# Optimization experiments

Hardware: AMD Instinct MI355X
Metric: run time of the kernel (lower is better)

## Reference

```python
import jax, jax.numpy as jnp
import numpy as np

B, D, H = 8192, 1024, 1024

def setup_inputs() -> dict:
    key = jax.random.key(0)
    ks = jax.random.split(key, 7)
    s_x = 1.0 / np.sqrt(D)
    s_h = 1.0 / np.sqrt(H)
    return {
        "e_t": jax.random.normal(ks[0], (B, D), jnp.float32),
        "h_prev": jax.random.normal(ks[1], (B, H), jnp.float32),
        "c_prev": jax.random.normal(ks[2], (B, H), jnp.float32),
        # gates concatenated in order (f, i, o, c), each block of size H
        "W_x": jax.random.uniform(ks[3], (4 * H, D), jnp.float32, -s_x, s_x),
        "b_x": jax.random.uniform(ks[4], (4 * H,), jnp.float32, -s_x, s_x),
        "W_h": jax.random.uniform(ks[5], (4 * H, H), jnp.float32, -s_h, s_h),
        "b_h": jax.random.uniform(ks[6], (4 * H,), jnp.float32, -s_h, s_h),
        "b_extra": jnp.zeros((4 * H,), jnp.float32),  # the b_f/b_i/b_o/b_c Parameters
    }

def reference(e_t, h_prev, c_prev, W_x, b_x, W_h, b_h, b_extra):
    # two fused GEMMs: [B,D]@[D,4H] and [B,H]@[H,4H]
    z = (jnp.einsum('bd,gd->bg', e_t, W_x)
         + jnp.einsum('bh,gh->bg', h_prev, W_h)
         + b_x + b_h + b_extra)  # [B, 4H]
    zf, zi, zo, zc = jnp.split(z, 4, axis=-1)
    g_t = jax.nn.sigmoid(zf)   # forget gate
    p_t = jax.nn.sigmoid(zi)   # input gate
    q_t = jax.nn.sigmoid(zo)   # output gate
    m_t_hat = jnp.tanh(zc)     # candidate cell
    c_t = g_t * c_prev + p_t * m_t_hat
    h_t = q_t * jnp.tanh(c_t)
    return (h_t, c_t)
```

## Files before the change

### kernel.cpp

```cpp
#include <hip/hip_runtime.h>
#include <stdint.h>

#define B_ROWS 8192
#define DH     1024
#define KTOT   2048
#define NTOT   4096

typedef __attribute__((ext_vector_type(8))) __bf16 bf16x8;
typedef __attribute__((ext_vector_type(4))) float  f32x4;

__device__ __forceinline__ unsigned short f2bf(float f) {
    unsigned int u = __float_as_uint(f);
    u += 0x7FFFu + ((u >> 16) & 1u);
    return (unsigned short)(u >> 16);
}

__device__ __forceinline__ float fast_sigmoid(float x) {
    return 1.0f / (1.0f + __expf(-x));
}
__device__ __forceinline__ float fast_tanh(float x) {
    float e = __expf(fminf(-2.0f * x, 80.0f));
    return (1.0f - e) / (1.0f + e);
}

#define NBLK_A (B_ROWS)
#define NBLK_W (NTOT)
#define NBLK_BIAS (NTOT / 256)

__global__ __launch_bounds__(256) void pack_all(const float* __restrict__ e_t,
                                                const float* __restrict__ h_prev,
                                                const float* __restrict__ W_x,
                                                const float* __restrict__ W_h,
                                                const float* __restrict__ b_x,
                                                const float* __restrict__ b_h,
                                                const float* __restrict__ b_e,
                                                unsigned short* __restrict__ A_cat,
                                                unsigned short* __restrict__ W_cat,
                                                float* __restrict__ bias) {
    const int blk = blockIdx.x;
    const int t   = threadIdx.x;
    if (blk < NBLK_A + NBLK_W) {
        const float* src0;
        unsigned short* dst;
        int row;
        if (blk < NBLK_A) {
            row = blk;
            dst = A_cat + (size_t)row * KTOT;
            int c8 = t << 3;
            src0 = (c8 < DH) ? (e_t + (size_t)row * DH + c8)
                             : (h_prev + (size_t)row * DH + (c8 - DH));
        } else {
            row = blk - NBLK_A;
            int gate = (row >> 4) & 3;
            int h    = (row >> 6) * 16 + (row & 15);
            int srow = gate * DH + h;
            dst = W_cat + (size_t)row * KTOT;
            int c8 = t << 3;
            src0 = (c8 < DH) ? (W_x + (size_t)srow * DH + c8)
                             : (W_h + (size_t)srow * DH + (c8 - DH));
        }
        float4 f0 = ((const float4*)src0)[0];
        float4 f1 = ((const float4*)src0)[1];
        uint4 o;
        o.x = (unsigned)f2bf(f0.x) | ((unsigned)f2bf(f0.y) << 16);
        o.y = (unsigned)f2bf(f0.z) | ((unsigned)f2bf(f0.w) << 16);
        o.z = (unsigned)f2bf(f1.x) | ((unsigned)f2bf(f1.y) << 16);
        o.w = (unsigned)f2bf(f1.z) | ((unsigned)f2bf(f1.w) << 16);
        *(uint4*)(dst + t * 8) = o;
    } else {
        int gp = (blk - NBLK_A - NBLK_W) * 256 + t;
        int gate = (gp >> 4) & 3;
        int h    = (gp >> 6) * 16 + (gp & 15);
        int g    = gate * DH + h;
        bias[gp] = b_x[g] + b_h[g] + b_e[g];
    }
}


#define GLL(srcp, dstp) \
    __builtin_amdgcn_global_load_lds( \
        (const __attribute__((address_space(1))) void*)(srcp), \
        (__attribute__((address_space(3))) void*)(dstp), 16, 0, 0)

#define STAGE_HALF(g, buf, h, kt) do { \
    GLL((g) + ((size_t)((h) * 128)      * KTOT) + (size_t)(kt) * 64, (buf) + (((h) * 128)      + w8) * 128); \
    GLL((g) + ((size_t)((h) * 128 + 64) * KTOT) + (size_t)(kt) * 64, (buf) + (((h) * 128 + 64) + w8) * 128); \
} while (0)

#define SB() __builtin_amdgcn_sched_barrier(0)

template <int MODE>
__device__ __forceinline__ void do_tile(
    int kt,
    unsigned char* As_cur, unsigned char* Bs_cur,
    const unsigned short* __restrict__ gA, const unsigned short* __restrict__ gB,
    int w8, int rowA, int rowB, int xg0, int xg1,
    f32x4 (&acc)[8][4])
{
    bf16x8 afl[4][2], afh[4][2], bfl[2][2], bfh[2][2];

#pragma unroll
    for (int mi = 0; mi < 4; ++mi) {
        afl[mi][0] = *(const bf16x8*)(As_cur + rowA + mi * 2048 + xg0);
        afl[mi][1] = *(const bf16x8*)(As_cur + rowA + mi * 2048 + xg1);
    }
#pragma unroll
    for (int ni = 0; ni < 2; ++ni) {
        bfl[ni][0] = *(const bf16x8*)(Bs_cur + rowB + ni * 2048 + xg0);
        bfl[ni][1] = *(const bf16x8*)(Bs_cur + rowB + ni * 2048 + xg1);
    }
    SB();
#pragma unroll
    for (int ni = 0; ni < 2; ++ni) {
        bfh[ni][0] = *(const bf16x8*)(Bs_cur + rowB + (2 + ni) * 2048 + xg0);
        bfh[ni][1] = *(const bf16x8*)(Bs_cur + rowB + (2 + ni) * 2048 + xg1);
    }
    SB();
#pragma unroll
    for (int mi = 0; mi < 4; ++mi) {
        afh[mi][0] = *(const bf16x8*)(As_cur + rowA + (4 + mi) * 2048 + xg0);
        afh[mi][1] = *(const bf16x8*)(As_cur + rowA + (4 + mi) * 2048 + xg1);
    }
    SB();

    asm volatile("s_waitcnt lgkmcnt(12)" ::: "memory");
    SB();
    __builtin_amdgcn_s_setprio(1);
#pragma unroll
    for (int mi = 0; mi < 4; ++mi)
#pragma unroll
        for (int ni = 0; ni < 2; ++ni) {
            acc[mi][ni] = __builtin_amdgcn_mfma_f32_16x16x32_bf16(afl[mi][0], bfl[ni][0], acc[mi][ni], 0, 0, 0);
            acc[mi][ni] = __builtin_amdgcn_mfma_f32_16x16x32_bf16(afl[mi][1], bfl[ni][1], acc[mi][ni], 0, 0, 0);
        }
    __builtin_amdgcn_s_setprio(0);
    SB();

    asm volatile("s_waitcnt lgkmcnt(8)" ::: "memory");
    SB();
    __builtin_amdgcn_s_setprio(1);
#pragma unroll
    for (int mi = 0; mi < 4; ++mi)
#pragma unroll
        for (int ni = 0; ni < 2; ++ni) {
            acc[mi][2 + ni] = __builtin_amdgcn_mfma_f32_16x16x32_bf16(afl[mi][0], bfh[ni][0], acc[mi][2 + ni], 0, 0, 0);
            acc[mi][2 + ni] = __builtin_amdgcn_mfma_f32_16x16x32_bf16(afl[mi][1], bfh[ni][1], acc[mi][2 + ni], 0, 0, 0);
        }
    __builtin_amdgcn_s_setprio(0);
    SB();

    asm volatile("s_waitcnt lgkmcnt(0)" ::: "memory");
    SB();
    if constexpr (MODE == 2) {
        __builtin_amdgcn_s_barrier();
        SB();
        STAGE_HALF(gB, Bs_cur, 0, kt + 2);
        STAGE_HALF(gB, Bs_cur, 1, kt + 2);
        STAGE_HALF(gA, As_cur, 0, kt + 2);
        STAGE_HALF(gA, As_cur, 1, kt + 2);
        SB();
    }

    __builtin_amdgcn_s_setprio(1);
#pragma unroll
    for (int mi = 0; mi < 4; ++mi)
#pragma unroll
        for (int ni = 0; ni < 2; ++ni) {
            acc[4 + mi][ni] = __builtin_amdgcn_mfma_f32_16x16x32_bf16(afh[mi][0], bfl[ni][0], acc[4 + mi][ni], 0, 0, 0);
            acc[4 + mi][ni] = __builtin_amdgcn_mfma_f32_16x16x32_bf16(afh[mi][1], bfl[ni][1], acc[4 + mi][ni], 0, 0, 0);
        }
    __builtin_amdgcn_s_setprio(0);

    __builtin_amdgcn_s_setprio(1);
#pragma unroll
    for (int mi = 0; mi < 4; ++mi)
#pragma unroll
        for (int ni = 0; ni < 2; ++ni) {
            acc[4 + mi][2 + ni] = __builtin_amdgcn_mfma_f32_16x16x32_bf16(afh[mi][0], bfh[ni][0], acc[4 + mi][2 + ni], 0, 0, 0);
            acc[4 + mi][2 + ni] = __builtin_amdgcn_mfma_f32_16x16x32_bf16(afh[mi][1], bfh[ni][1], acc[4 + mi][2 + ni], 0, 0, 0);
        }
    __builtin_amdgcn_s_setprio(0);
    SB();

    if constexpr (MODE == 2) {
        asm volatile("s_waitcnt vmcnt(8)" ::: "memory");
        SB();
        __builtin_amdgcn_s_barrier();
        SB();
    } else if constexpr (MODE == 1) {
        asm volatile("s_waitcnt vmcnt(0)" ::: "memory");
        SB();
        __builtin_amdgcn_s_barrier();
        SB();
    }
}

__global__ __launch_bounds__(512, 2) void lstm_gemm(
    const unsigned short* __restrict__ A,
    const unsigned short* __restrict__ Wc,
    const float* __restrict__ bias,
    const float* __restrict__ c_prev,
    float* __restrict__ h_out,
    float* __restrict__ c_out)
{
    __shared__ __align__(16) unsigned char lds[131072];

    const int tid = threadIdx.x;
    const int w   = tid >> 6;
    const int l   = tid & 63;
    const int wm  = w >> 2, wn = w & 3;
    const int m0  = blockIdx.y * 256;
    const int n0  = blockIdx.x * 256;
    const int w8  = w * 8;

    f32x4 acc[8][4];
#pragma unroll
    for (int i = 0; i < 8; ++i)
#pragma unroll
        for (int j = 0; j < 4; ++j) acc[i][j] = {0.f, 0.f, 0.f, 0.f};

    const int srow = w8 + (l >> 3);
    const int scol = ((l & 7) ^ ((l >> 3) & 7)) * 8;
    const unsigned short* gA = A  + (size_t)(m0 + srow) * KTOT + scol;
    const unsigned short* gB = Wc + (size_t)(n0 + srow) * KTOT + scol;

    unsigned char* As0 = lds;
    unsigned char* As1 = lds + 32768;
    unsigned char* Bs0 = lds + 65536;
    unsigned char* Bs1 = lds + 98304;

    const int lane15 = l & 15;
    const int quad   = l >> 4;
    const int rowA = (wm * 128 + lane15) * 128;
    const int rowB = (wn * 64  + lane15) * 128;
    const int xg0  = ((0 + quad) ^ (lane15 & 7)) * 16;
    const int xg1  = ((4 + quad) ^ (lane15 & 7)) * 16;

    STAGE_HALF(gA, As0, 0, 0);
    STAGE_HALF(gA, As0, 1, 0);
    STAGE_HALF(gB, Bs0, 0, 0);
    STAGE_HALF(gB, Bs0, 1, 0);
    STAGE_HALF(gA, As1, 0, 1);
    STAGE_HALF(gA, As1, 1, 1);
    STAGE_HALF(gB, Bs1, 0, 1);
    STAGE_HALF(gB, Bs1, 1, 1);
    SB();
    asm volatile("s_waitcnt vmcnt(8)" ::: "memory");
    SB();
    __builtin_amdgcn_s_barrier();
    SB();

#pragma unroll 1
    for (int kt2 = 0; kt2 < 15; ++kt2) {
        do_tile<2>(2 * kt2,     As0, Bs0, gA, gB, w8, rowA, rowB, xg0, xg1, acc);
        do_tile<2>(2 * kt2 + 1, As1, Bs1, gA, gB, w8, rowA, rowB, xg0, xg1, acc);
    }
    do_tile<1>(30, As0, Bs0, gA, gB, w8, rowA, rowB, xg0, xg1, acc);
    do_tile<0>(31, As1, Bs1, gA, gB, w8, rowA, rowB, xg0, xg1, acc);

    float biasv[4];
#pragma unroll
    for (int nj = 0; nj < 4; ++nj)
        biasv[nj] = bias[n0 + wn * 64 + nj * 16 + lane15];

    const int hcol = ((n0 + wn * 64) >> 6) * 16 + lane15;

#pragma unroll
    for (int mi = 0; mi < 8; ++mi) {
        const int mbase = m0 + wm * 128 + mi * 16 + quad * 4;
        f32x4 zf4 = acc[mi][0];
        f32x4 zi4 = acc[mi][1];
        f32x4 zo4 = acc[mi][2];
        f32x4 zc4 = acc[mi][3];
#pragma unroll
        for (int r = 0; r < 4; ++r) {
            float zf = zf4[r] + biasv[0];
            float zi = zi4[r] + biasv[1];
            float zo = zo4[r] + biasv[2];
            float zc = zc4[r] + biasv[3];

            float gf = fast_sigmoid(zf);
            float gi = fast_sigmoid(zi);
            float go = fast_sigmoid(zo);
            float mh = fast_tanh(zc);

            const size_t off = (size_t)(mbase + r) * DH + hcol;
            float cp = c_prev[off];
            float ct = gf * cp + gi * mh;
            float ht = go * fast_tanh(ct);
            h_out[off] = ht;
            c_out[off] = ct;
        }
    }
}

extern "C" void kernel_launch(void* const* d_in, const int* in_sizes, int n_in,
                              void* d_out, int out_size, void* d_ws, size_t ws_size,
                              hipStream_t stream) {
    const float* e_t     = (const float*)d_in[0];
    const float* h_prev  = (const float*)d_in[1];
    const float* c_prev  = (const float*)d_in[2];
    const float* W_x     = (const float*)d_in[3];
    const float* b_x     = (const float*)d_in[4];
    const float* W_h     = (const float*)d_in[5];
    const float* b_h     = (const float*)d_in[6];
    const float* b_extra = (const float*)d_in[7];

    float* h_out = (float*)d_out;
    float* c_out = h_out + (size_t)B_ROWS * DH;

    unsigned short* A_cat = (unsigned short*)d_ws;
    unsigned short* W_cat = (unsigned short*)((char*)d_ws + (size_t)B_ROWS * KTOT * 2);
    float*          bias  = (float*)((char*)d_ws + (size_t)B_ROWS * KTOT * 2 + (size_t)NTOT * KTOT * 2);

    pack_all<<<NBLK_A + NBLK_W + NBLK_BIAS, 256, 0, stream>>>(
        e_t, h_prev, W_x, W_h, b_x, b_h, b_extra, A_cat, W_cat, bias);
    lstm_gemm<<<dim3(NTOT / 256, B_ROWS / 256), 512, 0, stream>>>(
        A_cat, W_cat, bias, c_prev, h_out, c_out);
}
```

Baseline: 295.7 us.

## Split each K-tile into four barrier-synced phases with one-ahead A prefetch

```diff
diff --git a/kernel.cpp b/kernel.cpp
--- a/kernel.cpp
+++ b/kernel.cpp
@@ -89,110 +89,102 @@
 
 #define SB() __builtin_amdgcn_sched_barrier(0)
 
+#define PHASE_SYNC() do { \
+    SB(); \
+    __builtin_amdgcn_s_barrier(); \
+    asm volatile("s_waitcnt lgkmcnt(0)" ::: "memory"); \
+    SB(); \
+} while (0)
+
+#define PHASE_CLOSE() do { \
+    SB(); \
+    __builtin_amdgcn_s_barrier(); \
+    SB(); \
+} while (0)
+
 template <int MODE>
 __device__ __forceinline__ void do_tile(
     int kt,
-    unsigned char* As_cur, unsigned char* Bs_cur,
+    unsigned char* As_cur, unsigned char* As_next, unsigned char* Bs_cur,
     const unsigned short* __restrict__ gA, const unsigned short* __restrict__ gB,
     int w8, int rowA, int rowB, int xg0, int xg1,
     f32x4 (&acc)[8][4])
 {
-    bf16x8 afl[4][2], afh[4][2], bfl[2][2], bfh[2][2];
-
-#pragma unroll
-    for (int mi = 0; mi < 4; ++mi) {
-        afl[mi][0] = *(const bf16x8*)(As_cur + rowA + mi * 2048 + xg0);
-        afl[mi][1] = *(const bf16x8*)(As_cur + rowA + mi * 2048 + xg1);
-    }
-#pragma unroll
-    for (int ni = 0; ni < 2; ++ni) {
-        bfl[ni][0] = *(const bf16x8*)(Bs_cur + rowB + ni * 2048 + xg0);
-        bfl[ni][1] = *(const bf16x8*)(Bs_cur + rowB + ni * 2048 + xg1);
-    }
-    SB();
-#pragma unroll
-    for (int ni = 0; ni < 2; ++ni) {
-        bfh[ni][0] = *(const bf16x8*)(Bs_cur + rowB + (2 + ni) * 2048 + xg0);
-        bfh[ni][1] = *(const bf16x8*)(Bs_cur + rowB + (2 + ni) * 2048 + xg1);
-    }
-    SB();
-#pragma unroll
-    for (int mi = 0; mi < 4; ++mi) {
-        afh[mi][0] = *(const bf16x8*)(As_cur + rowA + (4 + mi) * 2048 + xg0);
-        afh[mi][1] = *(const bf16x8*)(As_cur + rowA + (4 + mi) * 2048 + xg1);
-    }
-    SB();
-
-    asm volatile("s_waitcnt lgkmcnt(12)" ::: "memory");
-    SB();
+    bf16x8 al[4], b[4];
+
+#pragma unroll
+    for (int mi = 0; mi < 4; ++mi)
+        al[mi] = *(const bf16x8*)(As_cur + rowA + mi * 2048 + xg0);
+#pragma unroll
+    for (int ni = 0; ni < 4; ++ni)
+        b[ni] = *(const bf16x8*)(Bs_cur + rowB + ni * 2048 + xg0);
+    if constexpr (MODE >= 1) STAGE_HALF(gA, As_next, 0, kt + 1);
+    PHASE_SYNC();
     __builtin_amdgcn_s_setprio(1);
 #pragma unroll
     for (int mi = 0; mi < 4; ++mi)
 #pragma unroll
-        for (int ni = 0; ni < 2; ++ni) {
-            acc[mi][ni] = __builtin_amdgcn_mfma_f32_16x16x32_bf16(afl[mi][0], bfl[ni][0], acc[mi][ni], 0, 0, 0);
-            acc[mi][ni] = __builtin_amdgcn_mfma_f32_16x16x32_bf16(afl[mi][1], bfl[ni][1], acc[mi][ni], 0, 0, 0);
-        }
+        for (int ni = 0; ni < 4; ++ni)
+            acc[mi][ni] = __builtin_amdgcn_mfma_f32_16x16x32_bf16(al[mi], b[ni], acc[mi][ni], 0, 0, 0);
     __builtin_amdgcn_s_setprio(0);
-    SB();
-
-    asm volatile("s_waitcnt lgkmcnt(8)" ::: "memory");
-    SB();
+    PHASE_CLOSE();
+
+    bf16x8 ah[4];
+#pragma unroll
+    for (int mi = 0; mi < 4; ++mi)
+        ah[mi] = *(const bf16x8*)(As_cur + rowA + (4 + mi) * 2048 + xg0);
+    if constexpr (MODE >= 1) STAGE_HALF(gA, As_next, 1, kt + 1);
+    PHASE_SYNC();
     __builtin_amdgcn_s_setprio(1);
 #pragma unroll
     for (int mi = 0; mi < 4; ++mi)
 #pragma unroll
-        for (int ni = 0; ni < 2; ++ni) {
-            acc[mi][2 + ni] = __builtin_amdgcn_mfma_f32_16x16x32_bf16(afl[mi][0], bfh[ni][0], acc[mi][2 + ni], 0, 0, 0);
-            acc[mi][2 + ni] = __builtin_amdgcn_mfma_f32_16x16x32_bf16(afl[mi][1], bfh[ni][1], acc[mi][2 + ni], 0, 0, 0);
-        }
+        for (int ni = 0; ni < 4; ++ni)
+            acc[4 + mi][ni] = __builtin_amdgcn_mfma_f32_16x16x32_bf16(ah[mi], b[ni], acc[4 + mi][ni], 0, 0, 0);
     __builtin_amdgcn_s_setprio(0);
-    SB();
-
-    asm volatile("s_waitcnt lgkmcnt(0)" ::: "memory");
-    SB();
+    PHASE_CLOSE();
+
+#pragma unroll
+    for (int mi = 0; mi < 4; ++mi)
+        al[mi] = *(const bf16x8*)(As_cur + rowA + mi * 2048 + xg1);
+#pragma unroll
+    for (int ni = 0; ni < 4; ++ni)
+        b[ni] = *(const bf16x8*)(Bs_cur + rowB + ni * 2048 + xg1);
+    PHASE_SYNC();
+    __builtin_amdgcn_s_setprio(1);
+#pragma unroll
+    for (int mi = 0; mi < 4; ++mi)
+#pragma unroll
+        for (int ni = 0; ni < 4; ++ni)
+            acc[mi][ni] = __builtin_amdgcn_mfma_f32_16x16x32_bf16(al[mi], b[ni], acc[mi][ni], 0, 0, 0);
+    __builtin_amdgcn_s_setprio(0);
+    PHASE_CLOSE();
+
+#pragma unroll
+    for (int mi = 0; mi < 4; ++mi)
+        ah[mi] = *(const bf16x8*)(As_cur + rowA + (4 + mi) * 2048 + xg1);
     if constexpr (MODE == 2) {
-        __builtin_amdgcn_s_barrier();
-        SB();
         STAGE_HALF(gB, Bs_cur, 0, kt + 2);
         STAGE_HALF(gB, Bs_cur, 1, kt + 2);
-        STAGE_HALF(gA, As_cur, 0, kt + 2);
-        STAGE_HALF(gA, As_cur, 1, kt + 2);
-        SB();
-    }
-
+    }
+    PHASE_SYNC();
     __builtin_amdgcn_s_setprio(1);
 #pragma unroll
     for (int mi = 0; mi < 4; ++mi)
 #pragma unroll
-        for (int ni = 0; ni < 2; ++ni) {
-            acc[4 + mi][ni] = __builtin_amdgcn_mfma_f32_16x16x32_bf16(afh[mi][0], bfl[ni][0], acc[4 + mi][ni], 0, 0, 0);
-            acc[4 + mi][ni] = __builtin_amdgcn_mfma_f32_16x16x32_bf16(afh[mi][1], bfl[ni][1], acc[4 + mi][ni], 0, 0, 0);
-        }
+        for (int ni = 0; ni < 4; ++ni)
+            acc[4 + mi][ni] = __builtin_amdgcn_mfma_f32_16x16x32_bf16(ah[mi], b[ni], acc[4 + mi][ni], 0, 0, 0);
     __builtin_amdgcn_s_setprio(0);
-
-    __builtin_amdgcn_s_setprio(1);
-#pragma unroll
-    for (int mi = 0; mi < 4; ++mi)
-#pragma unroll
-        for (int ni = 0; ni < 2; ++ni) {
-            acc[4 + mi][2 + ni] = __builtin_amdgcn_mfma_f32_16x16x32_bf16(afh[mi][0], bfh[ni][0], acc[4 + mi][2 + ni], 0, 0, 0);
-            acc[4 + mi][2 + ni] = __builtin_amdgcn_mfma_f32_16x16x32_bf16(afh[mi][1], bfh[ni][1], acc[4 + mi][2 + ni], 0, 0, 0);
-        }
-    __builtin_amdgcn_s_setprio(0);
-    SB();
-
+    SB();
     if constexpr (MODE == 2) {
-        asm volatile("s_waitcnt vmcnt(8)" ::: "memory");
-        SB();
-        __builtin_amdgcn_s_barrier();
+        asm volatile("s_waitcnt vmcnt(4)" ::: "memory");
         SB();
     } else if constexpr (MODE == 1) {
         asm volatile("s_waitcnt vmcnt(0)" ::: "memory");
         SB();
-        __builtin_amdgcn_s_barrier();
-        SB();
-    }
+    }
+    __builtin_amdgcn_s_barrier();
+    SB();
 }
 
 __global__ __launch_bounds__(512, 2) void lstm_gemm(
@@ -240,23 +232,21 @@
     STAGE_HALF(gA, As0, 1, 0);
     STAGE_HALF(gB, Bs0, 0, 0);
     STAGE_HALF(gB, Bs0, 1, 0);
-    STAGE_HALF(gA, As1, 0, 1);
-    STAGE_HALF(gA, As1, 1, 1);
     STAGE_HALF(gB, Bs1, 0, 1);
     STAGE_HALF(gB, Bs1, 1, 1);
     SB();
-    asm volatile("s_waitcnt vmcnt(8)" ::: "memory");
+    asm volatile("s_waitcnt vmcnt(4)" ::: "memory");
     SB();
     __builtin_amdgcn_s_barrier();
     SB();
 
 #pragma unroll 1
     for (int kt2 = 0; kt2 < 15; ++kt2) {
-        do_tile<2>(2 * kt2,     As0, Bs0, gA, gB, w8, rowA, rowB, xg0, xg1, acc);
-        do_tile<2>(2 * kt2 + 1, As1, Bs1, gA, gB, w8, rowA, rowB, xg0, xg1, acc);
-    }
-    do_tile<1>(30, As0, Bs0, gA, gB, w8, rowA, rowB, xg0, xg1, acc);
-    do_tile<0>(31, As1, Bs1, gA, gB, w8, rowA, rowB, xg0, xg1, acc);
+        do_tile<2>(2 * kt2,     As0, As1, Bs0, gA, gB, w8, rowA, rowB, xg0, xg1, acc);
+        do_tile<2>(2 * kt2 + 1, As1, As0, Bs1, gA, gB, w8, rowA, rowB, xg0, xg1, acc);
+    }
+    do_tile<1>(30, As0, As1, Bs0, gA, gB, w8, rowA, rowB, xg0, xg1, acc);
+    do_tile<0>(31, As1, As0, Bs1, gA, gB, w8, rowA, rowB, xg0, xg1, acc);
 
     float biasv[4];
 #pragma unroll
```

After: 303.9 us. 2.8% more time.
